# Kernel optimization log

Measured on AMD Instinct MI355X. Metric: run time of the kernel, lower is better.

The kernel has to match this reference:

```python
import jax, jax.numpy as jnp
import numpy as np

B, S, D, H = 4, 2048, 1024, 16
HD = D // H


def setup_inputs() -> dict:
    key = jax.random.key(0)
    ks = jax.random.split(key, 12)
    sc = 1.0 / np.sqrt(D)
    return {
        "x": jax.random.normal(ks[0], (B, S, D), dtype=jnp.float32),
        "key_padding_mask": jax.random.randint(ks[1], (B, S), 0, 2).astype(bool),
        "attn_mask_modifier": jax.random.uniform(ks[2], (B, S, S), dtype=jnp.float32),
        "Wq": jax.random.normal(ks[3], (D, D), dtype=jnp.float32) * sc,
        "bq": jax.random.normal(ks[4], (D,), dtype=jnp.float32) * sc,
        "Wk": jax.random.normal(ks[5], (D, D), dtype=jnp.float32) * sc,
        "bk": jax.random.normal(ks[6], (D,), dtype=jnp.float32) * sc,
        "Wv": jax.random.normal(ks[7], (D, D), dtype=jnp.float32) * sc,
        "bv": jax.random.normal(ks[8], (D,), dtype=jnp.float32) * sc,
        "Wo": jax.random.normal(ks[9], (D, D), dtype=jnp.float32) * sc,
        "bo": jax.random.normal(ks[10], (D,), dtype=jnp.float32) * sc,
    }


def reference(x, key_padding_mask, attn_mask_modifier, Wq, bq, Wk, bk, Wv, bv, Wo, bo):
    b, s, d = x.shape
    hd = d // H
    # QKV projections -> [b, H, s, hd]
    q = (x @ Wq + bq).reshape(b, s, H, hd).transpose(0, 2, 1, 3)
    k = (x @ Wk + bk).reshape(b, s, H, hd).transpose(0, 2, 1, 3)
    v = (x @ Wv + bv).reshape(b, s, H, hd).transpose(0, 2, 1, 3)
    energy = jnp.einsum("bhqd,bhkd->bhqk", q, k) / jnp.sqrt(jnp.asarray(hd, x.dtype))
    # handle_neg=False path: multiplicative mask modifier, broadcast over heads
    energy = energy * attn_mask_modifier[:, None, :, :]
    # key_padding_mask is applied on the QUERY axis (unsqueeze(1).unsqueeze(-1)) per source
    energy = jnp.where(key_padding_mask[:, None, :, None], jnp.asarray(-1e10, x.dtype), energy)
    attn = jax.nn.softmax(energy, axis=-1)
    out = jnp.einsum("bhqk,bhkd->bhqd", attn, v).transpose(0, 2, 1, 3).reshape(b, s, d)
    return out @ Wo + bo
```

## Files before the change

kernel.cpp:

```cpp
#include <hip/hip_runtime.h>
#include <cstddef>

constexpr int Bn  = 4;
constexpr int Sn  = 2048;
constexpr int Dn  = 1024;
constexpr int Hn  = 16;
constexpr int HDn = 64;

typedef __bf16 bf16;
typedef __attribute__((ext_vector_type(8))) __bf16 bf16x8;
typedef __attribute__((ext_vector_type(4))) __bf16 bf16x4;
typedef __attribute__((ext_vector_type(4))) float  f32x4;

__global__ __launch_bounds__(256) void conv_f32_bf16_k(
    const float* __restrict__ in, bf16* __restrict__ out, int n)
{
    int i = (blockIdx.x * 256 + threadIdx.x) * 4;
    if (i + 3 < n) {
        float4 v = *(const float4*)(in + i);
        bf16 o[4] = {(bf16)v.x, (bf16)v.y, (bf16)v.z, (bf16)v.w};
        *(ulong1*)(out + i) = *(ulong1*)o;
    }
}

__global__ __launch_bounds__(256) void conv_wt_k(
    const float* __restrict__ w0, const float* __restrict__ w1,
    const float* __restrict__ w2, const float* __restrict__ w3,
    bf16* __restrict__ o0, bf16* __restrict__ o1,
    bf16* __restrict__ o2, bf16* __restrict__ o3)
{
    const float* W = (blockIdx.z == 0) ? w0 : (blockIdx.z == 1) ? w1
                   : (blockIdx.z == 2) ? w2 : w3;
    bf16* O = (blockIdx.z == 0) ? o0 : (blockIdx.z == 1) ? o1
            : (blockIdx.z == 2) ? o2 : o3;
    __shared__ float t[64][65];
    const int tid = threadIdx.x;
    const int k0 = blockIdx.x * 64;
    const int n0 = blockIdx.y * 64;
    #pragma unroll
    for (int p = 0; p < 16; ++p) {
        const int idx = p * 256 + tid;
        const int r = idx >> 6, c = idx & 63;
        t[r][c] = W[(size_t)(k0 + r) * Dn + n0 + c];
    }
    __syncthreads();
    #pragma unroll
    for (int p = 0; p < 16; ++p) {
        const int idx = p * 256 + tid;
        const int r = idx >> 6, c = idx & 63;
        O[(size_t)(n0 + r) * Dn + k0 + c] = (bf16)t[c][r];
    }
}

template <int MODE>
__global__ __launch_bounds__(256) void gemm_bf16_k(
    const bf16* __restrict__ A, const bf16* __restrict__ Bt,
    const float* __restrict__ bias, void* __restrict__ outv)
{
    __shared__ __align__(16) bf16 As[64][72];
    __shared__ __align__(16) bf16 Bs[64][72];

    const int tid  = threadIdx.x;
    const int w    = tid >> 6;
    const int lane = tid & 63;
    const int quad = lane >> 4;
    const int l15  = lane & 15;
    const int m0   = blockIdx.x * 64;
    const int n0   = blockIdx.y * 64;

    f32x4 acc[4] = {};

    for (int k0 = 0; k0 < Dn; k0 += 64) {
        #pragma unroll
        for (int p = 0; p < 2; ++p) {
            const int c = p * 256 + tid;
            const int r = c >> 3, off = (c & 7) * 8;
            *(bf16x8*)&As[r][off] =
                *(const bf16x8*)(A + (size_t)(m0 + r) * Dn + k0 + off);
            *(bf16x8*)&Bs[r][off] =
                *(const bf16x8*)(Bt + (size_t)(n0 + r) * Dn + k0 + off);
        }
        __syncthreads();
        #pragma unroll
        for (int ks = 0; ks < 64; ks += 32) {
            bf16x8 af = *(const bf16x8*)&As[w * 16 + l15][ks + quad * 8];
            #pragma unroll
            for (int ct = 0; ct < 4; ++ct) {
                bf16x8 bfr = *(const bf16x8*)&Bs[ct * 16 + l15][ks + quad * 8];
                acc[ct] = __builtin_amdgcn_mfma_f32_16x16x32_bf16(af, bfr, acc[ct], 0, 0, 0);
            }
        }
        __syncthreads();
    }

    #pragma unroll
    for (int ct = 0; ct < 4; ++ct) {
        const int c = n0 + ct * 16 + l15;
        const float bv = bias[c];
        #pragma unroll
        for (int i = 0; i < 4; ++i) {
            const int m = m0 + w * 16 + quad * 4 + i;
            const float v = acc[ct][i] + bv;
            if (MODE == 0) {
                ((float*)outv)[(size_t)m * Dn + c] = v;
            } else {
                const int b = m >> 11, s = m & (Sn - 1);
                const int h = c >> 6, hd = c & 63;
                if (MODE == 1)
                    ((bf16*)outv)[(((size_t)(b * Hn + h) * Sn) + s) * HDn + hd] = (bf16)v;
                else
                    ((bf16*)outv)[(((size_t)(b * Hn + h) * HDn) + hd) * Sn + s] = (bf16)v;
            }
        }
    }
}

__global__ __launch_bounds__(256) void attn_mfma_k(
    const bf16* __restrict__ Qb, const bf16* __restrict__ Kb,
    const bf16* __restrict__ Vtb, const int* __restrict__ kpm,
    const float* __restrict__ mod, bf16* __restrict__ att)
{
    __shared__ __align__(16) bf16 Ks[64][72];
    __shared__ __align__(16) bf16 Vts[64][72];
    __shared__ __align__(16) bf16 Ps[64][72];

    const int tid  = threadIdx.x;
    const int w    = tid >> 6;
    const int lane = tid & 63;
    const int quad = lane >> 4;
    const int l15  = lane & 15;
    const int bh   = blockIdx.x;
    const int b    = bh >> 4;
    const int h    = bh & 15;
    const int q0   = blockIdx.y * 64;
    const size_t base = (size_t)bh * Sn * HDn;

    const int qrow = q0 + w * 16 + l15;
    const bf16x8 qf0 = *(const bf16x8*)(Qb + base + (size_t)qrow * HDn + 0  + quad * 8);
    const bf16x8 qf1 = *(const bf16x8*)(Qb + base + (size_t)qrow * HDn + 32 + quad * 8);

    const bool qm = kpm[(size_t)b * Sn + qrow] != 0;
    const float* modrow = mod + ((size_t)b * Sn + qrow) * Sn;

    constexpr float SC = 0.125f * 1.44269504088896340736f;

    float m_r = -1e30f;
    float l_r = 0.0f;
    f32x4 O[4] = {};

    for (int k0 = 0; k0 < Sn; k0 += 64) {
        #pragma unroll
        for (int p = 0; p < 2; ++p) {
            const int c = p * 256 + tid;
            const int r = c >> 3, off = (c & 7) * 8;
            *(bf16x8*)&Ks[r][off] =
                *(const bf16x8*)(Kb + base + (size_t)(k0 + r) * HDn + off);
            *(bf16x8*)&Vts[r][off] =
                *(const bf16x8*)(Vtb + base + (size_t)r * Sn + k0 + off);
        }
        float4 md[4];
        #pragma unroll
        for (int ct = 0; ct < 4; ++ct)
            md[ct] = *(const float4*)(modrow + k0 + ct * 16 + quad * 4);
        __syncthreads();

        float e[4][4];
        #pragma unroll
        for (int ct = 0; ct < 4; ++ct) {
            f32x4 s = {};
            #pragma unroll
            for (int ks = 0; ks < 64; ks += 32) {
                bf16x8 kf = *(const bf16x8*)&Ks[ct * 16 + l15][ks + quad * 8];
                s = __builtin_amdgcn_mfma_f32_16x16x32_bf16(kf, ks ? qf1 : qf0, s, 0, 0, 0);
            }
            #pragma unroll
            for (int i = 0; i < 4; ++i)
                e[ct][i] = qm ? -1e10f : s[i] * SC * (&md[ct].x)[i];
        }

        float pmax = e[0][0];
        #pragma unroll
        for (int ct = 0; ct < 4; ++ct)
            #pragma unroll
            for (int i = 0; i < 4; ++i)
                pmax = fmaxf(pmax, e[ct][i]);
        pmax = fmaxf(pmax, __shfl_xor(pmax, 16));
        pmax = fmaxf(pmax, __shfl_xor(pmax, 32));

        const float mnew  = fmaxf(m_r, pmax);
        const float alpha = __builtin_amdgcn_exp2f(m_r - mnew);
        m_r = mnew;

        float rs = 0.0f;
        #pragma unroll
        for (int ct = 0; ct < 4; ++ct) {
            bf16x4 pb;
            #pragma unroll
            for (int i = 0; i < 4; ++i) {
                const bf16 p = (bf16)__builtin_amdgcn_exp2f(e[ct][i] - mnew);
                pb[i] = p;
                rs += (float)p;
            }
            *(bf16x4*)&Ps[w * 16 + l15][ct * 16 + quad * 4] = pb;
        }
        rs += __shfl_xor(rs, 16);
        rs += __shfl_xor(rs, 32);
        l_r = l_r * alpha + rs;

        float aO[4];
        #pragma unroll
        for (int i = 0; i < 4; ++i)
            aO[i] = __shfl(alpha, quad * 4 + i, 16);
        #pragma unroll
        for (int ct = 0; ct < 4; ++ct)
            #pragma unroll
            for (int i = 0; i < 4; ++i)
                O[ct][i] *= aO[i];

        #pragma unroll
        for (int ks = 0; ks < 64; ks += 32) {
            bf16x8 paf = *(const bf16x8*)&Ps[w * 16 + l15][ks + quad * 8];
            #pragma unroll
            for (int ct = 0; ct < 4; ++ct) {
                bf16x8 vf = *(const bf16x8*)&Vts[ct * 16 + l15][ks + quad * 8];
                O[ct] = __builtin_amdgcn_mfma_f32_16x16x32_bf16(paf, vf, O[ct], 0, 0, 0);
            }
        }
        __syncthreads();
    }

    float lO[4];
    #pragma unroll
    for (int i = 0; i < 4; ++i)
        lO[i] = 1.0f / __shfl(l_r, quad * 4 + i, 16);
    #pragma unroll
    for (int ct = 0; ct < 4; ++ct)
        #pragma unroll
        for (int i = 0; i < 4; ++i) {
            const int row = q0 + w * 16 + quad * 4 + i;
            const int col = h * HDn + ct * 16 + l15;
            att[((size_t)b * Sn + row) * Dn + col] = (bf16)(O[ct][i] * lO[i]);
        }
}

extern "C" void kernel_launch(void* const* d_in, const int* in_sizes, int n_in,
                              void* d_out, int out_size, void* d_ws, size_t ws_size,
                              hipStream_t stream) {
    const float* x   = (const float*)d_in[0];
    const int*   kpm = (const int*)d_in[1];
    const float* mod = (const float*)d_in[2];
    const float* Wq  = (const float*)d_in[3];
    const float* bq  = (const float*)d_in[4];
    const float* Wk  = (const float*)d_in[5];
    const float* bk  = (const float*)d_in[6];
    const float* Wv  = (const float*)d_in[7];
    const float* bv  = (const float*)d_in[8];
    const float* Wo  = (const float*)d_in[9];
    const float* bo  = (const float*)d_in[10];
    float* out = (float*)d_out;

    bf16* ws = (bf16*)d_ws;
    const size_t sz = (size_t)Bn * Sn * Dn;
    const size_t wz = (size_t)Dn * Dn;
    bf16* xb   = ws;
    bf16* qb   = ws + sz;
    bf16* kb   = ws + 2 * sz;
    bf16* vtb  = ws + 3 * sz;
    bf16* attb = ws + 4 * sz;
    bf16* wqt  = ws + 5 * sz;
    bf16* wkt  = wqt + wz;
    bf16* wvt  = wkt + wz;
    bf16* wot  = wvt + wz;

    conv_f32_bf16_k<<<(int)(sz / 1024), 256, 0, stream>>>(x, xb, (int)sz);
    conv_wt_k<<<dim3(16, 16, 4), 256, 0, stream>>>(Wq, Wk, Wv, Wo, wqt, wkt, wvt, wot);

    const dim3 gemm_grid(128, 16);
    gemm_bf16_k<1><<<gemm_grid, 256, 0, stream>>>(xb, wqt, bq, qb);
    gemm_bf16_k<1><<<gemm_grid, 256, 0, stream>>>(xb, wkt, bk, kb);
    gemm_bf16_k<2><<<gemm_grid, 256, 0, stream>>>(xb, wvt, bv, vtb);

    attn_mfma_k<<<dim3(Bn * Hn, Sn / 64), 256, 0, stream>>>(qb, kb, vtb, kpm, mod, attb);

    gemm_bf16_k<0><<<gemm_grid, 256, 0, stream>>>(attb, wot, bo, out);
}
```

Baseline: 484.0 us.

## Enlarge GEMM tiles with direct-to-LDS loads and prefetch swizzled attention tiles

```diff
diff --git a/kernel.cpp b/kernel.cpp
--- a/kernel.cpp
+++ b/kernel.cpp
@@ -11,6 +11,9 @@
 typedef __attribute__((ext_vector_type(8))) __bf16 bf16x8;
 typedef __attribute__((ext_vector_type(4))) __bf16 bf16x4;
 typedef __attribute__((ext_vector_type(4))) float  f32x4;
+
+typedef __attribute__((address_space(1))) const void gvoid;
+typedef __attribute__((address_space(3))) void lvoid;
 
 __global__ __launch_bounds__(256) void conv_f32_bf16_k(
     const float* __restrict__ in, bf16* __restrict__ out, int n)
@@ -57,62 +60,84 @@
     const bf16* __restrict__ A, const bf16* __restrict__ Bt,
     const float* __restrict__ bias, void* __restrict__ outv)
 {
-    __shared__ __align__(16) bf16 As[64][72];
-    __shared__ __align__(16) bf16 Bs[64][72];
+    __shared__ __align__(16) bf16 As[128 * 64];
+    __shared__ __align__(16) bf16 Bs[128 * 64];
 
     const int tid  = threadIdx.x;
     const int w    = tid >> 6;
     const int lane = tid & 63;
     const int quad = lane >> 4;
     const int l15  = lane & 15;
-    const int m0   = blockIdx.x * 64;
-    const int n0   = blockIdx.y * 64;
-
-    f32x4 acc[4] = {};
+    const int m0   = blockIdx.x * 128;
+    const int n0   = blockIdx.y * 128;
+    const int wm   = w >> 1;
+    const int wn   = w & 1;
+
+    const int srow = lane >> 3;
+    const int scol = (lane & 7) * 8;
+
+    f32x4 acc[4][4] = {};
 
     for (int k0 = 0; k0 < Dn; k0 += 64) {
         #pragma unroll
-        for (int p = 0; p < 2; ++p) {
-            const int c = p * 256 + tid;
-            const int r = c >> 3, off = (c & 7) * 8;
-            *(bf16x8*)&As[r][off] =
-                *(const bf16x8*)(A + (size_t)(m0 + r) * Dn + k0 + off);
-            *(bf16x8*)&Bs[r][off] =
-                *(const bf16x8*)(Bt + (size_t)(n0 + r) * Dn + k0 + off);
+        for (int j = 0; j < 4; ++j) {
+            const int rbase = (w * 4 + j) * 8;
+            const int r = rbase + srow;
+            __builtin_amdgcn_global_load_lds(
+                (gvoid*)(A + (size_t)(m0 + r) * Dn + k0 + scol),
+                (lvoid*)&As[rbase * 64], 16, 0, 0);
+            __builtin_amdgcn_global_load_lds(
+                (gvoid*)(Bt + (size_t)(n0 + r) * Dn + k0 + scol),
+                (lvoid*)&Bs[rbase * 64], 16, 0, 0);
         }
         __syncthreads();
+
         #pragma unroll
         for (int ks = 0; ks < 64; ks += 32) {
-            bf16x8 af = *(const bf16x8*)&As[w * 16 + l15][ks + quad * 8];
-            #pragma unroll
-            for (int ct = 0; ct < 4; ++ct) {
-                bf16x8 bfr = *(const bf16x8*)&Bs[ct * 16 + l15][ks + quad * 8];
-                acc[ct] = __builtin_amdgcn_mfma_f32_16x16x32_bf16(af, bfr, acc[ct], 0, 0, 0);
-            }
+            bf16x8 af[4], bfr[4];
+            #pragma unroll
+            for (int fm = 0; fm < 4; ++fm)
+                af[fm] = *(const bf16x8*)&As[(wm * 64 + fm * 16 + l15) * 64 + ks + quad * 8];
+            #pragma unroll
+            for (int fn = 0; fn < 4; ++fn)
+                bfr[fn] = *(const bf16x8*)&Bs[(wn * 64 + fn * 16 + l15) * 64 + ks + quad * 8];
+            #pragma unroll
+            for (int fm = 0; fm < 4; ++fm)
+                #pragma unroll
+                for (int fn = 0; fn < 4; ++fn)
+                    acc[fm][fn] = __builtin_amdgcn_mfma_f32_16x16x32_bf16(
+                        af[fm], bfr[fn], acc[fm][fn], 0, 0, 0);
         }
         __syncthreads();
     }
 
     #pragma unroll
-    for (int ct = 0; ct < 4; ++ct) {
-        const int c = n0 + ct * 16 + l15;
+    for (int fn = 0; fn < 4; ++fn) {
+        const int c = n0 + wn * 64 + fn * 16 + l15;
         const float bv = bias[c];
         #pragma unroll
-        for (int i = 0; i < 4; ++i) {
-            const int m = m0 + w * 16 + quad * 4 + i;
-            const float v = acc[ct][i] + bv;
-            if (MODE == 0) {
-                ((float*)outv)[(size_t)m * Dn + c] = v;
-            } else {
-                const int b = m >> 11, s = m & (Sn - 1);
-                const int h = c >> 6, hd = c & 63;
-                if (MODE == 1)
-                    ((bf16*)outv)[(((size_t)(b * Hn + h) * Sn) + s) * HDn + hd] = (bf16)v;
-                else
-                    ((bf16*)outv)[(((size_t)(b * Hn + h) * HDn) + hd) * Sn + s] = (bf16)v;
-            }
-        }
-    }
+        for (int fm = 0; fm < 4; ++fm) {
+            #pragma unroll
+            for (int i = 0; i < 4; ++i) {
+                const int m = m0 + wm * 64 + fm * 16 + quad * 4 + i;
+                const float v = acc[fm][fn][i] + bv;
+                if (MODE == 0) {
+                    ((float*)outv)[(size_t)m * Dn + c] = v;
+                } else {
+                    const int b = m >> 11, s = m & (Sn - 1);
+                    const int h = c >> 6, hd = c & 63;
+                    if (MODE == 1)
+                        ((bf16*)outv)[(((size_t)(b * Hn + h) * Sn) + s) * HDn + hd] = (bf16)v;
+                    else
+                        ((bf16*)outv)[(((size_t)(b * Hn + h) * HDn) + hd) * Sn + s] = (bf16)v;
+                }
+            }
+        }
+    }
+}
+
+__device__ __forceinline__ int sidx(int r, int c) {
+    return r * 64 + (c ^ ((r & 7) << 3));
 }
 
 __global__ __launch_bounds__(256) void attn_mfma_k(
@@ -120,19 +145,20 @@
     const bf16* __restrict__ Vtb, const int* __restrict__ kpm,
     const float* __restrict__ mod, bf16* __restrict__ att)
 {
-    __shared__ __align__(16) bf16 Ks[64][72];
-    __shared__ __align__(16) bf16 Vts[64][72];
-    __shared__ __align__(16) bf16 Ps[64][72];
+    __shared__ __align__(16) bf16 Ks[64 * 64];
+    __shared__ __align__(16) bf16 Vts[64 * 64];
+    __shared__ __align__(16) bf16 Ps[64 * 64];
 
     const int tid  = threadIdx.x;
     const int w    = tid >> 6;
     const int lane = tid & 63;
     const int quad = lane >> 4;
     const int l15  = lane & 15;
-    const int bh   = blockIdx.x;
+    const int blk  = blockIdx.x;
+    const int bh   = blk >> 5;
+    const int q0   = (blk & 31) * 64;
     const int b    = bh >> 4;
     const int h    = bh & 15;
-    const int q0   = blockIdx.y * 64;
     const size_t base = (size_t)bh * Sn * HDn;
 
     const int qrow = q0 + w * 16 + l15;
@@ -148,21 +174,46 @@
     float l_r = 0.0f;
     f32x4 O[4] = {};
 
-    for (int k0 = 0; k0 < Sn; k0 += 64) {
-        #pragma unroll
-        for (int p = 0; p < 2; ++p) {
-            const int c = p * 256 + tid;
-            const int r = c >> 3, off = (c & 7) * 8;
-            *(bf16x8*)&Ks[r][off] =
-                *(const bf16x8*)(Kb + base + (size_t)(k0 + r) * HDn + off);
-            *(bf16x8*)&Vts[r][off] =
-                *(const bf16x8*)(Vtb + base + (size_t)r * Sn + k0 + off);
-        }
-        float4 md[4];
-        #pragma unroll
-        for (int ct = 0; ct < 4; ++ct)
-            md[ct] = *(const float4*)(modrow + k0 + ct * 16 + quad * 4);
-        __syncthreads();
+    int sr[2], soff[2];
+    #pragma unroll
+    for (int p = 0; p < 2; ++p) {
+        const int c = p * 256 + tid;
+        sr[p] = c >> 3; soff[p] = (c & 7) * 8;
+    }
+
+    bf16x8 kst[2], vst[2];
+    float4 md[4];
+    #pragma unroll
+    for (int p = 0; p < 2; ++p) {
+        kst[p] = *(const bf16x8*)(Kb + base + (size_t)sr[p] * HDn + soff[p]);
+        vst[p] = *(const bf16x8*)(Vtb + base + (size_t)sr[p] * Sn + 0 + soff[p]);
+    }
+    #pragma unroll
+    for (int ct = 0; ct < 4; ++ct)
+        md[ct] = *(const float4*)(modrow + 0 + ct * 16 + quad * 4);
+    #pragma unroll
+    for (int p = 0; p < 2; ++p) {
+        *(bf16x8*)&Ks[sidx(sr[p], soff[p])]  = kst[p];
+        *(bf16x8*)&Vts[sidx(sr[p], soff[p])] = vst[p];
+    }
+    __syncthreads();
+
+    constexpr int NT = Sn / 64;
+    for (int t = 0; t < NT; ++t) {
+        const int k0 = t * 64;
+
+        float4 mdn[4];
+        if (t + 1 < NT) {
+            const int kn = k0 + 64;
+            #pragma unroll
+            for (int p = 0; p < 2; ++p) {
+                kst[p] = *(const bf16x8*)(Kb + base + (size_t)(kn + sr[p]) * HDn + soff[p]);
+                vst[p] = *(const bf16x8*)(Vtb + base + (size_t)sr[p] * Sn + kn + soff[p]);
+            }
+            #pragma unroll
+            for (int ct = 0; ct < 4; ++ct)
+                mdn[ct] = *(const float4*)(modrow + kn + ct * 16 + quad * 4);
+        }
 
         float e[4][4];
         #pragma unroll
@@ -170,7 +221,7 @@
             f32x4 s = {};
             #pragma unroll
             for (int ks = 0; ks < 64; ks += 32) {
-                bf16x8 kf = *(const bf16x8*)&Ks[ct * 16 + l15][ks + quad * 8];
+                bf16x8 kf = *(const bf16x8*)&Ks[sidx(ct * 16 + l15, ks + quad * 8)];
                 s = __builtin_amdgcn_mfma_f32_16x16x32_bf16(kf, ks ? qf1 : qf0, s, 0, 0, 0);
             }
             #pragma unroll
@@ -201,7 +252,7 @@
                 pb[i] = p;
                 rs += (float)p;
             }
-            *(bf16x4*)&Ps[w * 16 + l15][ct * 16 + quad * 4] = pb;
+            *(bf16x4*)&Ps[sidx(w * 16 + l15, ct * 16 + quad * 4)] = pb;
         }
         rs += __shfl_xor(rs, 16);
         rs += __shfl_xor(rs, 32);
@@ -219,12 +270,24 @@
 
         #pragma unroll
         for (int ks = 0; ks < 64; ks += 32) {
-            bf16x8 paf = *(const bf16x8*)&Ps[w * 16 + l15][ks + quad * 8];
+            bf16x8 paf = *(const bf16x8*)&Ps[sidx(w * 16 + l15, ks + quad * 8)];
             #pragma unroll
             for (int ct = 0; ct < 4; ++ct) {
-                bf16x8 vf = *(const bf16x8*)&Vts[ct * 16 + l15][ks + quad * 8];
+                bf16x8 vf = *(const bf16x8*)&Vts[sidx(ct * 16 + l15, ks + quad * 8)];
                 O[ct] = __builtin_amdgcn_mfma_f32_16x16x32_bf16(paf, vf, O[ct], 0, 0, 0);
             }
+        }
+
+        __syncthreads();
+        if (t + 1 < NT) {
+            #pragma unroll
+            for (int p = 0; p < 2; ++p) {
+                *(bf16x8*)&Ks[sidx(sr[p], soff[p])]  = kst[p];
+                *(bf16x8*)&Vts[sidx(sr[p], soff[p])] = vst[p];
+            }
+            #pragma unroll
+            for (int ct = 0; ct < 4; ++ct)
+                md[ct] = mdn[ct];
         }
         __syncthreads();
     }
@@ -275,12 +338,12 @@
     conv_f32_bf16_k<<<(int)(sz / 1024), 256, 0, stream>>>(x, xb, (int)sz);
     conv_wt_k<<<dim3(16, 16, 4), 256, 0, stream>>>(Wq, Wk, Wv, Wo, wqt, wkt, wvt, wot);
 
-    const dim3 gemm_grid(128, 16);
+    const dim3 gemm_grid(64, 8);
     gemm_bf16_k<1><<<gemm_grid, 256, 0, stream>>>(xb, wqt, bq, qb);
     gemm_bf16_k<1><<<gemm_grid, 256, 0, stream>>>(xb, wkt, bk, kb);
     gemm_bf16_k<2><<<gemm_grid, 256, 0, stream>>>(xb, wvt, bv, vtb);
 
-    attn_mfma_k<<<dim3(Bn * Hn, Sn / 64), 256, 0, stream>>>(qb, kb, vtb, kpm, mod, attb);
+    attn_mfma_k<<<Bn * Hn * (Sn / 64), 256, 0, stream>>>(qb, kb, vtb, kpm, mod, attb);
 
     gemm_bf16_k<0><<<gemm_grid, 256, 0, stream>>>(attb, wot, bo, out);
 }
```

After: 437.4 us. -9.6%, faster.
